# Performance work log

Hardware: AMD Instinct MI355X
Metric: run time of the kernel (lower is better)

## Reference

```python
import jax, jax.numpy as jnp
import numpy as np

B, N, IN, H, D = 4096, 65536, 64, 512, 256  # samples, total neighbors, input_size, hidden_size, dist_dim
EMB_IN = IN + H + D  # 832, social_emb Linear input dim


def setup_inputs() -> dict:
    key = jax.random.key(0)
    ks = jax.random.split(key, 12)
    # contiguous ragged segments tiling [0, N): random sorted boundaries
    boundaries = jnp.sort(jax.random.randint(ks[0], (B - 1,), 0, N, dtype=jnp.int32))
    starts = jnp.concatenate([jnp.zeros((1,), jnp.int32), boundaries])
    ends = jnp.concatenate([boundaries, jnp.full((1,), N, jnp.int32)])
    s = 0.02
    return {
        "traj_input": jax.random.normal(ks[1], (B, H), jnp.float32),
        "neighbor_t": jax.random.normal(ks[2], (N, IN), jnp.float32),
        "dist": jax.random.normal(ks[3], (N, D), jnp.float32),
        "ht": jax.random.normal(ks[4], (N, H), jnp.float32),
        "W_emb": jax.random.normal(ks[5], (EMB_IN, H), jnp.float32) * s,
        "b_emb": jnp.zeros((H,), jnp.float32),
        "w_ih": jax.random.normal(ks[6], (3 * H, H), jnp.float32) * s,
        "w_hh": jax.random.normal(ks[7], (3 * H, H), jnp.float32) * s,
        "b_ih": jnp.zeros((3 * H,), jnp.float32),
        "b_hh": jnp.zeros((3 * H,), jnp.float32),
        "neighbors_idx_start": starts,
        "neighbors_idx_end": ends,
    }


def reference(traj_input, neighbor_t, dist, ht, W_emb, b_emb, w_ih, w_hh, b_ih, b_hh,
              neighbors_idx_start, neighbors_idx_end):
    Nn = neighbor_t.shape[0]
    # map each flat neighbor row to its owning sample (segments are contiguous & sorted)
    sample_id = jnp.searchsorted(neighbors_idx_start, jnp.arange(Nn, dtype=neighbors_idx_start.dtype), side='right') - 1
    # ragged gather + concat: [N, IN + H + D]
    x = jnp.concatenate([neighbor_t, traj_input[sample_id], dist], axis=-1)
    emb = jax.nn.relu(x @ W_emb + b_emb)  # social_emb: Linear + ReLU
    # PyTorch GRUCell math
    gi = emb @ w_ih.T + b_ih  # [N, 3H]
    gh = ht @ w_hh.T + b_hh   # [N, 3H]
    i_r, i_z, i_n = jnp.split(gi, 3, axis=-1)
    h_r, h_z, h_n = jnp.split(gh, 3, axis=-1)
    r = jax.nn.sigmoid(i_r + h_r)
    z = jax.nn.sigmoid(i_z + h_z)
    n = jnp.tanh(i_n + r * h_n)
    return (1.0 - z) * n + z * ht  # [N, H], concat of per-sample GRU outputs
```

## Files before the change

kernel.cpp:

```cpp
#include <hip/hip_runtime.h>
#include <stdint.h>

#define BSAMP 4096
#define NTOT  65536
#define INW   64
#define HW    512
#define DW    256
#define EMB_IN 832

typedef unsigned short ushort_t;
using bf16x8 = __attribute__((ext_vector_type(8))) short;
using f32x4  = __attribute__((ext_vector_type(4))) float;

__device__ __forceinline__ ushort_t f2bf(float f) {
    unsigned int x = __builtin_bit_cast(unsigned int, f);
    x = x + 0x7fff + ((x >> 16) & 1);
    return (ushort_t)(x >> 16);
}

__device__ __forceinline__ void async16(const void* g, void* l) {
    __builtin_amdgcn_global_load_lds((const __attribute__((address_space(1))) unsigned int*)g,
                                     (__attribute__((address_space(3))) unsigned int*)l,
                                     16, 0, 0);
}

__global__ __launch_bounds__(256) void k_cvt(const float* __restrict__ in,
                                             ushort_t* __restrict__ out, int n) {
    int i = blockIdx.x * 256 + threadIdx.x;
    if (i < n) out[i] = f2bf(in[i]);
}

__global__ __launch_bounds__(256) void k_transpose(const float* __restrict__ in,
                                                   ushort_t* __restrict__ out) {
    int i = blockIdx.x * 256 + threadIdx.x;
    if (i >= HW * EMB_IN) return;
    int n = i / EMB_IN;
    int k = i - n * EMB_IN;
    out[i] = f2bf(in[k * HW + n]);
}

__global__ __launch_bounds__(256) void k_build_wrz(const float* __restrict__ wih,
                                                   const float* __restrict__ whh,
                                                   ushort_t* __restrict__ wrz) {
    int i = blockIdx.x * 256 + threadIdx.x;
    int row = i >> 10, k = i & 1023;
    float v = (k < 512) ? wih[row * 512 + k] : whh[row * 512 + (k - 512)];
    wrz[i] = f2bf(v);
}

__global__ __launch_bounds__(256) void k_build_wnn(const float* __restrict__ wih,
                                                   const float* __restrict__ whh,
                                                   ushort_t* __restrict__ wnn) {
    int i = blockIdx.x * 256 + threadIdx.x;
    int h = i >> 10, k = i & 1023;
    float v = (k < 512) ? wih[(1024 + h) * 512 + k] : whh[(1024 + h) * 512 + (k - 512)];
    wnn[i] = f2bf(v);
}

__global__ __launch_bounds__(256) void k_sid(const int* __restrict__ starts,
                                             int* __restrict__ sid) {
    int n = blockIdx.x * 256 + threadIdx.x;
    int lo = 0, hi = BSAMP - 1;
    #pragma unroll
    for (int it = 0; it < 12; ++it) {
        int mid = (lo + hi + 1) >> 1;
        if (starts[mid] <= n) lo = mid; else hi = mid - 1;
    }
    sid[n] = lo;
}

__global__ __launch_bounds__(256) void k_cvt_ht(const float* __restrict__ ht,
                                                ushort_t* __restrict__ Acat, int n128) {
    int i = blockIdx.x * 256 + threadIdx.x;
    if (i >= n128) return;
    int row = i >> 7, c4 = i & 127;
    float4 v = *(const float4*)(ht + row * 512 + c4 * 4);
    ushort_t* d = Acat + (size_t)row * 1024 + 512 + c4 * 4;
    d[0] = f2bf(v.x); d[1] = f2bf(v.y); d[2] = f2bf(v.z); d[3] = f2bf(v.w);
}

__global__ __launch_bounds__(256) void k_emb(const float* __restrict__ neigh,
                                             const ushort_t* __restrict__ trajbf,
                                             const float* __restrict__ dist,
                                             const ushort_t* __restrict__ wembT,
                                             const float* __restrict__ bemb,
                                             const int* __restrict__ sid,
                                             ushort_t* __restrict__ Acat,
                                             int base) {
    __shared__ short As[128 * 64];
    __shared__ short Bs[128 * 64];

    const int tid = threadIdx.x;
    const int cb = blockIdx.x, rb = blockIdx.y;
    const int lrow0 = rb * 128;
    const int row0g = base + lrow0;
    const int wave = tid >> 6, lane = tid & 63;
    const int wm = wave & 1, wn = wave >> 1;
    const int quad = lane >> 4, l15 = lane & 15;
    const int mb = wm * 64, nb = wn * 64;
    const int srow = lane >> 3, sc8 = lane & 7;
    const int swz = (l15 & 7) << 3;

    f32x4 acc[4][4];
    #pragma unroll
    for (int i = 0; i < 4; ++i)
        #pragma unroll
        for (int j = 0; j < 4; ++j) acc[i][j] = (f32x4){0.f, 0.f, 0.f, 0.f};

    for (int kk = 0; kk < 13; ++kk) {
        #pragma unroll
        for (int p = 0; p < 4; ++p) {
            int row = p * 32 + wave * 8 + srow;
            async16(wembT + (cb * 128 + row) * EMB_IN + kk * 64 + (sc8 ^ srow) * 8,
                    &Bs[p * 2048 + wave * 512]);
        }
        if (kk == 0) {
            #pragma unroll
            for (int p = 0; p < 8; ++p) {
                int idx = p * 256 + tid;
                int row = idx >> 4, c4 = idx & 15;
                float4 v = *(const float4*)(neigh + (row0g + row) * INW + c4 * 4);
                ushort_t* d = (ushort_t*)&As[row * 64 + ((c4 * 4) ^ ((row & 7) << 3))];
                d[0] = f2bf(v.x); d[1] = f2bf(v.y); d[2] = f2bf(v.z); d[3] = f2bf(v.w);
            }
        } else if (kk <= 8) {
            #pragma unroll
            for (int p = 0; p < 4; ++p) {
                int row = p * 32 + wave * 8 + srow;
                int s = sid[row0g + row];
                async16(trajbf + s * HW + (kk - 1) * 64 + (sc8 ^ srow) * 8,
                        &As[p * 2048 + wave * 512]);
            }
        } else {
            #pragma unroll
            for (int p = 0; p < 8; ++p) {
                int idx = p * 256 + tid;
                int row = idx >> 4, c4 = idx & 15;
                float4 v = *(const float4*)(dist + (row0g + row) * DW + (kk - 9) * 64 + c4 * 4);
                ushort_t* d = (ushort_t*)&As[row * 64 + ((c4 * 4) ^ ((row & 7) << 3))];
                d[0] = f2bf(v.x); d[1] = f2bf(v.y); d[2] = f2bf(v.z); d[3] = f2bf(v.w);
            }
        }
        __syncthreads();

        #pragma unroll
        for (int ks = 0; ks < 2; ++ks) {
            const int kb = (ks * 32 + quad * 8) ^ swz;
            bf16x8 af[4], bfr[4];
            #pragma unroll
            for (int i = 0; i < 4; ++i)
                af[i] = *(const bf16x8*)(&As[(mb + i * 16 + l15) * 64 + kb]);
            #pragma unroll
            for (int j = 0; j < 4; ++j)
                bfr[j] = *(const bf16x8*)(&Bs[(nb + j * 16 + l15) * 64 + kb]);
            #pragma unroll
            for (int i = 0; i < 4; ++i)
                #pragma unroll
                for (int j = 0; j < 4; ++j)
                    acc[i][j] = __builtin_amdgcn_mfma_f32_16x16x32_bf16(af[i], bfr[j], acc[i][j], 0, 0, 0);
        }
        __syncthreads();
    }

    #pragma unroll
    for (int j = 0; j < 4; ++j) {
        int gn = cb * 128 + nb + j * 16 + l15;
        float bias = bemb[gn];
        #pragma unroll
        for (int i = 0; i < 4; ++i) {
            int lm0 = lrow0 + mb + i * 16 + quad * 4;
            #pragma unroll
            for (int r = 0; r < 4; ++r) {
                float v = acc[i][j][r] + bias;
                v = v > 0.f ? v : 0.f;
                Acat[(size_t)(lm0 + r) * 1024 + gn] = f2bf(v);
            }
        }
    }
}

__global__ __launch_bounds__(256, 2) void k_gru(const ushort_t* __restrict__ Acat,
                                                const float* __restrict__ ht,
                                                const ushort_t* __restrict__ wrz,
                                                const ushort_t* __restrict__ wnn,
                                                const float* __restrict__ bih,
                                                const float* __restrict__ bhh,
                                                float* __restrict__ out,
                                                int base) {
    __shared__ short As[128 * 64];
    __shared__ short Bs[3 * 64 * 64];

    const int tid = threadIdx.x;
    const int hb = blockIdx.x, rb = blockIdx.y;
    const int lrow0 = rb * 128;
    const int row0g = base + lrow0;
    const int h0 = hb * 64;
    const int wave = tid >> 6, lane = tid & 63;
    const int wm = wave & 1, wn = wave >> 1;
    const int quad = lane >> 4, l15 = lane & 15;
    const int mb = wm * 64, nb = wn * 32;
    const int srow = lane >> 3, sc8 = lane & 7;
    const int swz = (l15 & 7) << 3;

    f32x4 accR[4][2], accZ[4][2], accNI[4][2], accNH[4][2];
    #pragma unroll
    for (int i = 0; i < 4; ++i)
        #pragma unroll
        for (int j = 0; j < 2; ++j) {
            accR[i][j] = (f32x4){0.f, 0.f, 0.f, 0.f};
            accZ[i][j] = (f32x4){0.f, 0.f, 0.f, 0.f};
            accNI[i][j] = (f32x4){0.f, 0.f, 0.f, 0.f};
            accNH[i][j] = (f32x4){0.f, 0.f, 0.f, 0.f};
        }

    const ushort_t* Wr = wrz + (size_t)h0 * 1024;
    const ushort_t* Wz = wrz + (size_t)(512 + h0) * 1024;
    const ushort_t* Wn = wnn + (size_t)h0 * 1024;

    auto body = [&](int kk, f32x4 (&accN)[4][2]) {
        #pragma unroll
        for (int p = 0; p < 4; ++p) {
            int row = p * 32 + wave * 8 + srow;
            async16(Acat + (size_t)(lrow0 + row) * 1024 + kk * 64 + (sc8 ^ srow) * 8,
                    &As[p * 2048 + wave * 512]);
        }
        #pragma unroll
        for (int p = 0; p < 2; ++p) {
            int row = p * 32 + wave * 8 + srow;
            int goff = row * 1024 + kk * 64 + (sc8 ^ srow) * 8;
            int loff = p * 2048 + wave * 512;
            async16(Wr + goff, &Bs[loff]);
            async16(Wz + goff, &Bs[4096 + loff]);
            async16(Wn + goff, &Bs[8192 + loff]);
        }
        __syncthreads();

        #pragma unroll
        for (int ks = 0; ks < 2; ++ks) {
            const int kb = (ks * 32 + quad * 8) ^ swz;
            bf16x8 af[4];
            #pragma unroll
            for (int i = 0; i < 4; ++i)
                af[i] = *(const bf16x8*)(&As[(mb + i * 16 + l15) * 64 + kb]);

            bf16x8 br0 = *(const bf16x8*)(&Bs[(nb + l15) * 64 + kb]);
            bf16x8 br1 = *(const bf16x8*)(&Bs[(nb + 16 + l15) * 64 + kb]);
            #pragma unroll
            for (int i = 0; i < 4; ++i) {
                accR[i][0] = __builtin_amdgcn_mfma_f32_16x16x32_bf16(af[i], br0, accR[i][0], 0, 0, 0);
                accR[i][1] = __builtin_amdgcn_mfma_f32_16x16x32_bf16(af[i], br1, accR[i][1], 0, 0, 0);
            }
            bf16x8 bz0 = *(const bf16x8*)(&Bs[4096 + (nb + l15) * 64 + kb]);
            bf16x8 bz1 = *(const bf16x8*)(&Bs[4096 + (nb + 16 + l15) * 64 + kb]);
            #pragma unroll
            for (int i = 0; i < 4; ++i) {
                accZ[i][0] = __builtin_amdgcn_mfma_f32_16x16x32_bf16(af[i], bz0, accZ[i][0], 0, 0, 0);
                accZ[i][1] = __builtin_amdgcn_mfma_f32_16x16x32_bf16(af[i], bz1, accZ[i][1], 0, 0, 0);
            }
            bf16x8 bn0 = *(const bf16x8*)(&Bs[8192 + (nb + l15) * 64 + kb]);
            bf16x8 bn1 = *(const bf16x8*)(&Bs[8192 + (nb + 16 + l15) * 64 + kb]);
            #pragma unroll
            for (int i = 0; i < 4; ++i) {
                accN[i][0] = __builtin_amdgcn_mfma_f32_16x16x32_bf16(af[i], bn0, accN[i][0], 0, 0, 0);
                accN[i][1] = __builtin_amdgcn_mfma_f32_16x16x32_bf16(af[i], bn1, accN[i][1], 0, 0, 0);
            }
        }
        __syncthreads();
    };

    for (int kk = 0; kk < 8; ++kk)  body(kk, accNI);
    for (int kk = 8; kk < 16; ++kk) body(kk, accNH);

    #pragma unroll
    for (int j = 0; j < 2; ++j) {
        int gn = h0 + nb + j * 16 + l15;
        float br = bih[gn] + bhh[gn];
        float bz = bih[gn + 512] + bhh[gn + 512];
        float bin = bih[gn + 1024], bhn = bhh[gn + 1024];
        #pragma unroll
        for (int i = 0; i < 4; ++i) {
            int gm0 = row0g + mb + i * 16 + quad * 4;
            #pragma unroll
            for (int r = 0; r < 4; ++r) {
                int gm = gm0 + r;
                float rg = 1.f / (1.f + __expf(-(accR[i][j][r] + br)));
                float zg = 1.f / (1.f + __expf(-(accZ[i][j][r] + bz)));
                float ng = tanhf(accNI[i][j][r] + bin + rg * (accNH[i][j][r] + bhn));
                float hp = ht[(size_t)gm * HW + gn];
                out[(size_t)gm * HW + gn] = (1.f - zg) * ng + zg * hp;
            }
        }
    }
}

extern "C" void kernel_launch(void* const* d_in, const int* in_sizes, int n_in,
                              void* d_out, int out_size, void* d_ws, size_t ws_size,
                              hipStream_t stream) {
    const float* traj   = (const float*)d_in[0];
    const float* neigh  = (const float*)d_in[1];
    const float* dist   = (const float*)d_in[2];
    const float* ht     = (const float*)d_in[3];
    const float* W_emb  = (const float*)d_in[4];
    const float* b_emb  = (const float*)d_in[5];
    const float* w_ih   = (const float*)d_in[6];
    const float* w_hh   = (const float*)d_in[7];
    const float* b_ih   = (const float*)d_in[8];
    const float* b_hh   = (const float*)d_in[9];
    const int*   starts = (const int*)d_in[10];

    char* ws = (char*)d_ws;
    int*      sid    = (int*)ws;
    ushort_t* wembT  = (ushort_t*)(ws + 262144);
    ushort_t* wrz    = (ushort_t*)(ws + 1114112);
    ushort_t* wnn    = (ushort_t*)(ws + 3211264);
    ushort_t* trajbf = (ushort_t*)(ws + 4259840);
    ushort_t* Acat   = (ushort_t*)(ws + 8454144);

    float* out = (float*)d_out;

    long long avail = (long long)ws_size - 8454144LL;
    int chunk_rows = (int)(avail / 2048);
    chunk_rows &= ~127;
    if (chunk_rows > NTOT) chunk_rows = NTOT;
    if (chunk_rows < 128) chunk_rows = 128;

    k_sid<<<dim3(NTOT / 256), dim3(256), 0, stream>>>(starts, sid);
    k_cvt<<<dim3((BSAMP * HW + 255) / 256), dim3(256), 0, stream>>>(traj, trajbf, BSAMP * HW);
    k_transpose<<<dim3((HW * EMB_IN + 255) / 256), dim3(256), 0, stream>>>(W_emb, wembT);
    k_build_wrz<<<dim3(1024 * 1024 / 256), dim3(256), 0, stream>>>(w_ih, w_hh, wrz);
    k_build_wnn<<<dim3(512 * 1024 / 256), dim3(256), 0, stream>>>(w_ih, w_hh, wnn);

    for (int base = 0; base < NTOT; base += chunk_rows) {
        int rows = NTOT - base;
        if (rows > chunk_rows) rows = chunk_rows;
        int n128 = rows * 128;
        k_cvt_ht<<<dim3((n128 + 255) / 256), dim3(256), 0, stream>>>(ht + (size_t)base * HW, Acat, n128);
        k_emb<<<dim3(4, rows / 128), dim3(256), 0, stream>>>(neigh, trajbf, dist, wembT,
                                                             b_emb, sid, Acat, base);
        k_gru<<<dim3(8, rows / 128), dim3(256), 0, stream>>>(Acat, ht, wrz, wnn,
                                                             b_ih, b_hh, out, base);
    }
}
```

Before: 764.5 us.

## Double-buffer LDS in emb and GRU GEMMs, pre-convert inputs to bf16, swizzle block order

Both GEMM kernels now use two LDS buffers and issue async loads for the next K-slice while MFMAs run on the current one, with s_setprio raised around the compute. The neighbor and distance inputs are converted to bf16 up front, so the emb kernel can load every A tile with async global-to-LDS copies instead of doing float loads and conversion in the loop. Grids are flattened to 1D with an XCD-style block remap so that blocks sharing weights or rows run close together. The cost is extra preprocessing passes, a larger workspace that may shrink the chunk size, and doubled LDS that may lower occupancy.

```diff
diff --git a/kernel.cpp b/kernel.cpp
--- a/kernel.cpp
+++ b/kernel.cpp
@@ -24,10 +24,15 @@
                                      16, 0, 0);
 }
 
-__global__ __launch_bounds__(256) void k_cvt(const float* __restrict__ in,
-                                             ushort_t* __restrict__ out, int n) {
-    int i = blockIdx.x * 256 + threadIdx.x;
-    if (i < n) out[i] = f2bf(in[i]);
+__global__ __launch_bounds__(256) void k_cvt4(const float* __restrict__ in,
+                                              ushort_t* __restrict__ out, int n4) {
+    int i = blockIdx.x * 256 + threadIdx.x;
+    if (i >= n4) return;
+    float4 v = *(const float4*)(in + (size_t)i * 4);
+    uint2 o;
+    o.x = (unsigned)f2bf(v.x) | ((unsigned)f2bf(v.y) << 16);
+    o.y = (unsigned)f2bf(v.z) | ((unsigned)f2bf(v.w) << 16);
+    *(uint2*)(out + (size_t)i * 4) = o;
 }
 
 __global__ __launch_bounds__(256) void k_transpose(const float* __restrict__ in,
@@ -79,19 +84,22 @@
     d[0] = f2bf(v.x); d[1] = f2bf(v.y); d[2] = f2bf(v.z); d[3] = f2bf(v.w);
 }
 
-__global__ __launch_bounds__(256) void k_emb(const float* __restrict__ neigh,
-                                             const ushort_t* __restrict__ trajbf,
-                                             const float* __restrict__ dist,
-                                             const ushort_t* __restrict__ wembT,
-                                             const float* __restrict__ bemb,
-                                             const int* __restrict__ sid,
-                                             ushort_t* __restrict__ Acat,
-                                             int base) {
-    __shared__ short As[128 * 64];
-    __shared__ short Bs[128 * 64];
+__global__ __launch_bounds__(256, 2) void k_emb(const ushort_t* __restrict__ neighbf,
+                                                const ushort_t* __restrict__ trajbf,
+                                                const ushort_t* __restrict__ distbf,
+                                                const ushort_t* __restrict__ wembT,
+                                                const float* __restrict__ bemb,
+                                                const int* __restrict__ sid,
+                                                ushort_t* __restrict__ Acat,
+                                                int base) {
+    __shared__ short As[2][128 * 64];
+    __shared__ short Bs[2][128 * 64];
 
     const int tid = threadIdx.x;
-    const int cb = blockIdx.x, rb = blockIdx.y;
+    const int b = blockIdx.x;
+    const int total = gridDim.x;
+    const int lg = (b & 7) * (total >> 3) + (b >> 3);
+    const int cb = lg & 3, rb = lg >> 2;
     const int lrow0 = rb * 128;
     const int row0g = base + lrow0;
     const int wave = tid >> 6, lane = tid & 63;
@@ -107,58 +115,54 @@
         #pragma unroll
         for (int j = 0; j < 4; ++j) acc[i][j] = (f32x4){0.f, 0.f, 0.f, 0.f};
 
-    for (int kk = 0; kk < 13; ++kk) {
+    auto stage = [&](int kk, int buf) {
         #pragma unroll
         for (int p = 0; p < 4; ++p) {
             int row = p * 32 + wave * 8 + srow;
             async16(wembT + (cb * 128 + row) * EMB_IN + kk * 64 + (sc8 ^ srow) * 8,
-                    &Bs[p * 2048 + wave * 512]);
-        }
-        if (kk == 0) {
-            #pragma unroll
-            for (int p = 0; p < 8; ++p) {
-                int idx = p * 256 + tid;
-                int row = idx >> 4, c4 = idx & 15;
-                float4 v = *(const float4*)(neigh + (row0g + row) * INW + c4 * 4);
-                ushort_t* d = (ushort_t*)&As[row * 64 + ((c4 * 4) ^ ((row & 7) << 3))];
-                d[0] = f2bf(v.x); d[1] = f2bf(v.y); d[2] = f2bf(v.z); d[3] = f2bf(v.w);
-            }
-        } else if (kk <= 8) {
-            #pragma unroll
-            for (int p = 0; p < 4; ++p) {
-                int row = p * 32 + wave * 8 + srow;
-                int s = sid[row0g + row];
-                async16(trajbf + s * HW + (kk - 1) * 64 + (sc8 ^ srow) * 8,
-                        &As[p * 2048 + wave * 512]);
-            }
-        } else {
-            #pragma unroll
-            for (int p = 0; p < 8; ++p) {
-                int idx = p * 256 + tid;
-                int row = idx >> 4, c4 = idx & 15;
-                float4 v = *(const float4*)(dist + (row0g + row) * DW + (kk - 9) * 64 + c4 * 4);
-                ushort_t* d = (ushort_t*)&As[row * 64 + ((c4 * 4) ^ ((row & 7) << 3))];
-                d[0] = f2bf(v.x); d[1] = f2bf(v.y); d[2] = f2bf(v.z); d[3] = f2bf(v.w);
-            }
-        }
-        __syncthreads();
-
+                    &Bs[buf][p * 2048 + wave * 512]);
+        }
+        #pragma unroll
+        for (int p = 0; p < 4; ++p) {
+            int row = p * 32 + wave * 8 + srow;
+            const ushort_t* src;
+            if (kk == 0)
+                src = neighbf + (size_t)(row0g + row) * 64 + (sc8 ^ srow) * 8;
+            else if (kk <= 8)
+                src = trajbf + (size_t)sid[row0g + row] * HW + (kk - 1) * 64 + (sc8 ^ srow) * 8;
+            else
+                src = distbf + (size_t)(row0g + row) * 256 + (kk - 9) * 64 + (sc8 ^ srow) * 8;
+            async16(src, &As[buf][p * 2048 + wave * 512]);
+        }
+    };
+
+    auto compute = [&](int buf) {
+        __builtin_amdgcn_s_setprio(1);
         #pragma unroll
         for (int ks = 0; ks < 2; ++ks) {
             const int kb = (ks * 32 + quad * 8) ^ swz;
             bf16x8 af[4], bfr[4];
             #pragma unroll
             for (int i = 0; i < 4; ++i)
-                af[i] = *(const bf16x8*)(&As[(mb + i * 16 + l15) * 64 + kb]);
+                af[i] = *(const bf16x8*)(&As[buf][(mb + i * 16 + l15) * 64 + kb]);
             #pragma unroll
             for (int j = 0; j < 4; ++j)
-                bfr[j] = *(const bf16x8*)(&Bs[(nb + j * 16 + l15) * 64 + kb]);
+                bfr[j] = *(const bf16x8*)(&Bs[buf][(nb + j * 16 + l15) * 64 + kb]);
             #pragma unroll
             for (int i = 0; i < 4; ++i)
                 #pragma unroll
                 for (int j = 0; j < 4; ++j)
                     acc[i][j] = __builtin_amdgcn_mfma_f32_16x16x32_bf16(af[i], bfr[j], acc[i][j], 0, 0, 0);
         }
+        __builtin_amdgcn_s_setprio(0);
+    };
+
+    stage(0, 0);
+    __syncthreads();
+    for (int kk = 0; kk < 13; ++kk) {
+        int buf = kk & 1;
+        if (kk < 12) stage(kk + 1, buf ^ 1);
+        compute(buf);
         __syncthreads();
     }
 
@@ -187,11 +191,14 @@
                                                 const float* __restrict__ bhh,
                                                 float* __restrict__ out,
                                                 int base) {
-    __shared__ short As[128 * 64];
-    __shared__ short Bs[3 * 64 * 64];
+    __shared__ short As[2][128 * 64];
+    __shared__ short Bs[2][3 * 64 * 64];
 
     const int tid = threadIdx.x;
-    const int hb = blockIdx.x, rb = blockIdx.y;
+    const int b = blockIdx.x;
+    const int total = gridDim.x;
+    const int lg = (b & 7) * (total >> 3) + (b >> 3);
+    const int hb = lg & 7, rb = lg >> 3;
     const int lrow0 = rb * 128;
     const int row0g = base + lrow0;
     const int h0 = hb * 64;
@@ -217,59 +224,73 @@
     const ushort_t* Wz = wrz + (size_t)(512 + h0) * 1024;
     const ushort_t* Wn = wnn + (size_t)h0 * 1024;
 
-    auto body = [&](int kk, f32x4 (&accN)[4][2]) {
+    auto stage = [&](int kk, int buf) {
         #pragma unroll
         for (int p = 0; p < 4; ++p) {
             int row = p * 32 + wave * 8 + srow;
             async16(Acat + (size_t)(lrow0 + row) * 1024 + kk * 64 + (sc8 ^ srow) * 8,
-                    &As[p * 2048 + wave * 512]);
+                    &As[buf][p * 2048 + wave * 512]);
         }
         #pragma unroll
         for (int p = 0; p < 2; ++p) {
             int row = p * 32 + wave * 8 + srow;
             int goff = row * 1024 + kk * 64 + (sc8 ^ srow) * 8;
             int loff = p * 2048 + wave * 512;
-            async16(Wr + goff, &Bs[loff]);
-            async16(Wz + goff, &Bs[4096 + loff]);
-            async16(Wn + goff, &Bs[8192 + loff]);
-        }
-        __syncthreads();
-
+            async16(Wr + goff, &Bs[buf][loff]);
+            async16(Wz + goff, &Bs[buf][4096 + loff]);
+            async16(Wn + goff, &Bs[buf][8192 + loff]);
+        }
+    };
+
+    auto compute = [&](int buf, f32x4 (&accN)[4][2]) {
+        __builtin_amdgcn_s_setprio(1);
         #pragma unroll
         for (int ks = 0; ks < 2; ++ks) {
             const int kb = (ks * 32 + quad * 8) ^ swz;
             bf16x8 af[4];
             #pragma unroll
             for (int i = 0; i < 4; ++i)
-                af[i] = *(const bf16x8*)(&As[(mb + i * 16 + l15) * 64 + kb]);
-
-            bf16x8 br0 = *(const bf16x8*)(&Bs[(nb + l15) * 64 + kb]);
-            bf16x8 br1 = *(const bf16x8*)(&Bs[(nb + 16 + l15) * 64 + kb]);
+                af[i] = *(const bf16x8*)(&As[buf][(mb + i * 16 + l15) * 64 + kb]);
+
+            bf16x8 br0 = *(const bf16x8*)(&Bs[buf][(nb + l15) * 64 + kb]);
+            bf16x8 br1 = *(const bf16x8*)(&Bs[buf][(nb + 16 + l15) * 64 + kb]);
             #pragma unroll
             for (int i = 0; i < 4; ++i) {
                 accR[i][0] = __builtin_amdgcn_mfma_f32_16x16x32_bf16(af[i], br0, accR[i][0], 0, 0, 0);
                 accR[i][1] = __builtin_amdgcn_mfma_f32_16x16x32_bf16(af[i], br1, accR[i][1], 0, 0, 0);
             }
-            bf16x8 bz0 = *(const bf16x8*)(&Bs[4096 + (nb + l15) * 64 + kb]);
-            bf16x8 bz1 = *(const bf16x8*)(&Bs[4096 + (nb + 16 + l15) * 64 + kb]);
+            bf16x8 bz0 = *(const bf16x8*)(&Bs[buf][4096 + (nb + l15) * 64 + kb]);
+            bf16x8 bz1 = *(const bf16x8*)(&Bs[buf][4096 + (nb + 16 + l15) * 64 + kb]);
             #pragma unroll
             for (int i = 0; i < 4; ++i) {
                 accZ[i][0] = __builtin_amdgcn_mfma_f32_16x16x32_bf16(af[i], bz0, accZ[i][0], 0, 0, 0);
                 accZ[i][1] = __builtin_amdgcn_mfma_f32_16x16x32_bf16(af[i], bz1, accZ[i][1], 0, 0, 0);
             }
-            bf16x8 bn0 = *(const bf16x8*)(&Bs[8192 + (nb + l15) * 64 + kb]);
-            bf16x8 bn1 = *(const bf16x8*)(&Bs[8192 + (nb + 16 + l15) * 64 + kb]);
+            bf16x8 bn0 = *(const bf16x8*)(&Bs[buf][8192 + (nb + l15) * 64 + kb]);
+            bf16x8 bn1 = *(const bf16x8*)(&Bs[buf][8192 + (nb + 16 + l15) * 64 + kb]);
             #pragma unroll
             for (int i = 0; i < 4; ++i) {
                 accN[i][0] = __builtin_amdgcn_mfma_f32_16x16x32_bf16(af[i], bn0, accN[i][0], 0, 0, 0);
                 accN[i][1] = __builtin_amdgcn_mfma_f32_16x16x32_bf16(af[i], bn1, accN[i][1], 0, 0, 0);
             }
         }
+        __builtin_amdgcn_s_setprio(0);
+    };
+
+    stage(0, 0);
+    __syncthreads();
+    for (int kk = 0; kk < 8; ++kk) {
+        int buf = kk & 1;
+        stage(kk + 1, buf ^ 1);
+        compute(buf, accNI);
         __syncthreads();
-    };
-
-    for (int kk = 0; kk < 8; ++kk)  body(kk, accNI);
-    for (int kk = 8; kk < 16; ++kk) body(kk, accNH);
+    }
+    for (int kk = 8; kk < 16; ++kk) {
+        int buf = kk & 1;
+        if (kk < 15) stage(kk + 1, buf ^ 1);
+        compute(buf, accNH);
+        __syncthreads();
+    }
 
     #pragma unroll
     for (int j = 0; j < 2; ++j) {
@@ -309,23 +330,27 @@
     const int*   starts = (const int*)d_in[10];
 
     char* ws = (char*)d_ws;
-    int*      sid    = (int*)ws;
-    ushort_t* wembT  = (ushort_t*)(ws + 262144);
-    ushort_t* wrz    = (ushort_t*)(ws + 1114112);
-    ushort_t* wnn    = (ushort_t*)(ws + 3211264);
-    ushort_t* trajbf = (ushort_t*)(ws + 4259840);
-    ushort_t* Acat   = (ushort_t*)(ws + 8454144);
+    int*      sid     = (int*)ws;
+    ushort_t* wembT   = (ushort_t*)(ws + 262144);
+    ushort_t* wrz     = (ushort_t*)(ws + 1114112);
+    ushort_t* wnn     = (ushort_t*)(ws + 3211264);
+    ushort_t* trajbf  = (ushort_t*)(ws + 4259840);
+    ushort_t* neighbf = (ushort_t*)(ws + 8454144);
+    ushort_t* distbf  = (ushort_t*)(ws + 16842752);
+    ushort_t* Acat    = (ushort_t*)(ws + 50397184);
 
     float* out = (float*)d_out;
 
-    long long avail = (long long)ws_size - 8454144LL;
+    long long avail = (long long)ws_size - 50397184LL;
     int chunk_rows = (int)(avail / 2048);
-    chunk_rows &= ~127;
+    chunk_rows &= ~255;
     if (chunk_rows > NTOT) chunk_rows = NTOT;
-    if (chunk_rows < 128) chunk_rows = 128;
+    if (chunk_rows < 256) chunk_rows = 256;
 
     k_sid<<<dim3(NTOT / 256), dim3(256), 0, stream>>>(starts, sid);
-    k_cvt<<<dim3((BSAMP * HW + 255) / 256), dim3(256), 0, stream>>>(traj, trajbf, BSAMP * HW);
+    k_cvt4<<<dim3(BSAMP * HW / 1024), dim3(256), 0, stream>>>(traj, trajbf, BSAMP * HW / 4);
+    k_cvt4<<<dim3(NTOT * INW / 1024), dim3(256), 0, stream>>>(neigh, neighbf, NTOT * INW / 4);
+    k_cvt4<<<dim3(NTOT * DW / 1024), dim3(256), 0, stream>>>(dist, distbf, NTOT * DW / 4);
     k_transpose<<<dim3((HW * EMB_IN + 255) / 256), dim3(256), 0, stream>>>(W_emb, wembT);
     k_build_wrz<<<dim3(1024 * 1024 / 256), dim3(256), 0, stream>>>(w_ih, w_hh, wrz);
     k_build_wnn<<<dim3(512 * 1024 / 256), dim3(256), 0, stream>>>(w_ih, w_hh, wnn);
@@ -335,9 +360,9 @@
         if (rows > chunk_rows) rows = chunk_rows;
         int n128 = rows * 128;
         k_cvt_ht<<<dim3((n128 + 255) / 256), dim3(256), 0, stream>>>(ht + (size_t)base * HW, Acat, n128);
-        k_emb<<<dim3(4, rows / 128), dim3(256), 0, stream>>>(neigh, trajbf, dist, wembT,
-                                                             b_emb, sid, Acat, base);
-        k_gru<<<dim3(8, rows / 128), dim3(256), 0, stream>>>(Acat, ht, wrz, wnn,
-                                                             b_ih, b_hh, out, base);
-    }
-}
+        k_emb<<<dim3(4 * (rows / 128)), dim3(256), 0, stream>>>(neighbf, trajbf, distbf, wembT,
+                                                                b_emb, sid, Acat, base);
+        k_gru<<<dim3(8 * (rows / 128)), dim3(256), 0, stream>>>(Acat, ht, wrz, wnn,
+                                                                b_ih, b_hh, out, base);
+    }
+}
```

New measurement: 729.5 us. 4.6% less time.
